# Kernel tuning notes

Hardware: AMD Instinct MI355X
Metric: run time of the kernel (lower is better)

Reference implementation:

```python
import jax, jax.numpy as jnp
import numpy as np
import math

B, T, C = 2, 2048, 1024
H, DK, DV = 16, 64, 64


def setup_inputs() -> dict:
    key = jax.random.key(0)
    ks = jax.random.split(key, 5)
    # randw(*d) = randn(*d) / sqrt(d[-1])
    x = jax.random.normal(ks[0], (B, T, C), dtype=jnp.float32)
    w_q = jax.random.normal(ks[1], (H, DK, C), dtype=jnp.float32) / math.sqrt(C)
    w_k = jax.random.normal(ks[2], (H, DK, C), dtype=jnp.float32) / math.sqrt(C)
    w_v = jax.random.normal(ks[3], (H, DV, C), dtype=jnp.float32) / math.sqrt(C)
    w_o = jax.random.normal(ks[4], (H * DV, C), dtype=jnp.float32) / math.sqrt(C)
    return {"x": x, "w_q": w_q, "w_k": w_k, "w_v": w_v, "w_o": w_o}


def reference(x, w_q, w_k, w_v, w_o):
    # Full prefill: bs_q.first = 0, bs_q.nb = T, causal=True, dropout=0 (eval).
    dk = w_q.shape[1]
    q = jnp.einsum('ntc,hdc->nhtd', x, w_q)  # [B,H,T,DK]
    k = jnp.einsum('ntc,hdc->nhtd', x, w_k)  # [B,H,T,DK]
    v = jnp.einsum('ntc,hdc->nhtd', x, w_v)  # [B,H,T,DV]
    a = jnp.einsum('nhtd,nhsd->nhts', q, k) / jnp.sqrt(jnp.asarray(dk, x.dtype))
    # amm_generator: mask where query_idx < key_idx (strict upper triangle)
    t = a.shape[-1]
    mask = jnp.arange(t)[:, None] < jnp.arange(t)[None, :]  # [T,T] bool
    a = jnp.where(mask[None, None], jnp.asarray(-jnp.inf, a.dtype), a)
    a = jax.nn.softmax(a, axis=-1)
    y = jnp.einsum('nhts,nhsd->nthd', a, v)  # [B,T,H,DV]
    y = y.reshape(y.shape[0], y.shape[1], -1)  # [B,T,H*DV]
    return y @ w_o  # [B,T,C]
```

## Files before the change

### kernel.cpp

```cpp
#include <hip/hip_runtime.h>
#include <hip/hip_bf16.h>

#define B_ 2
#define T_ 2048
#define C_ 1024
#define H_ 16
#define D_ 64

typedef __attribute__((ext_vector_type(8))) short bf16x8;
typedef __attribute__((ext_vector_type(4))) float f32x4;
typedef __attribute__((ext_vector_type(8))) unsigned short u16x8;
typedef __attribute__((ext_vector_type(2))) unsigned int u32x2;
typedef __attribute__((ext_vector_type(4))) unsigned int u32x4;

__device__ __forceinline__ unsigned short bf1(float a) {
    __bf16 x = (__bf16)a;
    return __builtin_bit_cast(unsigned short, x);
}
__device__ __forceinline__ unsigned int pk2(float a, float b) {
    return (unsigned int)bf1(a) | ((unsigned int)bf1(b) << 16);
}
__device__ __forceinline__ float bf2f(unsigned short u) {
    union { unsigned int u; float f; } v; v.u = (unsigned int)u << 16;
    return v.f;
}

__device__ __forceinline__ void gll16(const void* g, void* l) {
    __builtin_amdgcn_global_load_lds(
        (const __attribute__((address_space(1))) unsigned int*)g,
        (__attribute__((address_space(3))) unsigned int*)l, 16, 0, 0);
}

__global__ __launch_bounds__(256) void prep_x(
    const float* __restrict__ x, unsigned short* __restrict__ xb)
{
    const size_t i = ((size_t)blockIdx.x * 256 + threadIdx.x) * 16;
    float4 f0 = *reinterpret_cast<const float4*>(x + i);
    float4 f1 = *reinterpret_cast<const float4*>(x + i + 4);
    float4 f2 = *reinterpret_cast<const float4*>(x + i + 8);
    float4 f3 = *reinterpret_cast<const float4*>(x + i + 12);
    u32x4 a = {pk2(f0.x, f0.y), pk2(f0.z, f0.w), pk2(f1.x, f1.y), pk2(f1.z, f1.w)};
    u32x4 b = {pk2(f2.x, f2.y), pk2(f2.z, f2.w), pk2(f3.x, f3.y), pk2(f3.z, f3.w)};
    *reinterpret_cast<u32x4*>(xb + i) = a;
    *reinterpret_cast<u32x4*>(xb + i + 8) = b;
}

__global__ __launch_bounds__(256) void prep_w(
    const float* __restrict__ wq, const float* __restrict__ wk,
    const float* __restrict__ wv, unsigned short* __restrict__ wb)
{
    const int bid = blockIdx.x, tid = threadIdx.x;
    const int rb = bid * 4;
    const float* src = (rb < 1024) ? wq + (size_t)rb * 1024
                     : (rb < 2048) ? wk + (size_t)(rb - 1024) * 1024
                                   : wv + (size_t)(rb - 2048) * 1024;
    const float sc = (rb < 1024) ? 0.125f * 1.4426950408889634f : 1.0f;
    const float4* s4 = (const float4*)src;
    u32x2* d = (u32x2*)(wb + (size_t)rb * 1024);
#pragma unroll
    for (int k = 0; k < 4; k++) {
        float4 v = s4[k * 256 + tid];
        u32x2 w;
        w[0] = pk2(v.x * sc, v.y * sc);
        w[1] = pk2(v.z * sc, v.w * sc);
        d[k * 256 + tid] = w;
    }
}

__global__ __launch_bounds__(256) void prep_wo(
    const float* __restrict__ wo, unsigned short* __restrict__ wt)
{
    __shared__ unsigned short tile[64][72];
    const int tk = (blockIdx.x & 15) << 6, tn = (blockIdx.x >> 4) << 6;
    const int r = threadIdx.x >> 2, cb = (threadIdx.x & 3) << 4;
#pragma unroll
    for (int j = 0; j < 4; j++) {
        float4 v = *reinterpret_cast<const float4*>(
            wo + (size_t)(tk + r) * 1024 + tn + cb + j * 4);
        u32x2 w;
        w[0] = pk2(v.x, v.y);
        w[1] = pk2(v.z, v.w);
        *reinterpret_cast<u32x2*>(&tile[r][cb + j * 4]) = w;
    }
    __syncthreads();
    unsigned short buf[16];
#pragma unroll
    for (int j = 0; j < 16; j++) buf[j] = tile[cb + j][r];
    unsigned short* dst = wt + (size_t)(tn + r) * 1024 + tk + cb;
    *reinterpret_cast<u16x8*>(dst) = *reinterpret_cast<u16x8*>(buf);
    *reinterpret_cast<u16x8*>(dst + 8) = *reinterpret_cast<u16x8*>(buf + 8);
}

__global__ __launch_bounds__(256) void qkv_gemm(
    const unsigned short* __restrict__ xb, const unsigned short* __restrict__ wb,
    unsigned short* __restrict__ qkv)
{
    __shared__ __align__(16) unsigned short As[128 * 32];
    __shared__ __align__(16) unsigned short Bs[128 * 32];
    const int tid = threadIdx.x;
    const int lane = tid & 63, wave = tid >> 6;
    const int g = lane >> 4, c16 = lane & 15;
    const int xcd = blockIdx.x & 7, idx = blockIdx.x >> 3;
    const int bm = (xcd << 2) + idx / 24, bn = idx % 24;
    const int jbase = bn << 7;
    const int which = jbase >> 10;

    const int srow = lane >> 2, sch = (lane & 3) << 3;
    const unsigned short* asrc = xb + ((size_t)(bm << 7) + wave * 32 + srow) * C_ + sch;
    const unsigned short* bsrc = wb + ((size_t)(bn << 7) + wave * 32 + srow) * C_ + sch;

    f32x4 acc[4][4];
#pragma unroll
    for (int i = 0; i < 4; i++)
#pragma unroll
        for (int j = 0; j < 4; j++) acc[i][j] = (f32x4){0.f, 0.f, 0.f, 0.f};

    const int wm = (wave >> 1) << 6, wn = (wave & 1) << 6;

    for (int t = 0; t < 32; ++t) {
        const int k0 = t << 5;
        __syncthreads();
        gll16(asrc + k0,           &As[(wave * 32) << 5]);
        gll16(asrc + k0 + 16 * C_, &As[(wave * 32 + 16) << 5]);
        gll16(bsrc + k0,           &Bs[(wave * 32) << 5]);
        gll16(bsrc + k0 + 16 * C_, &Bs[(wave * 32 + 16) << 5]);
        __syncthreads();

        bf16x8 af[4], bfv[4];
#pragma unroll
        for (int m = 0; m < 4; m++)
            af[m] = *reinterpret_cast<const bf16x8*>(&As[((wm + m * 16 + c16) << 5) + g * 8]);
#pragma unroll
        for (int n = 0; n < 4; n++)
            bfv[n] = *reinterpret_cast<const bf16x8*>(&Bs[((wn + n * 16 + c16) << 5) + g * 8]);
#pragma unroll
        for (int m = 0; m < 4; m++)
#pragma unroll
            for (int n = 0; n < 4; n++)
                acc[m][n] = __builtin_amdgcn_mfma_f32_16x16x32_bf16(af[m], bfv[n], acc[m][n], 0, 0, 0);
    }

    if (which < 2) {
#pragma unroll
        for (int m = 0; m < 4; m++) {
            const int grow = (bm << 7) + wm + m * 16 + (g << 2);
#pragma unroll
            for (int n = 0; n < 4; n++) {
                const int jj = (jbase + wn + n * 16 + c16) & 1023;
                const int h = jj >> 6, d = jj & 63;
#pragma unroll
                for (int r = 0; r < 4; r++) {
                    const int row = grow + r;
                    const int b = row >> 11, t = row & 2047;
                    const size_t off = ((size_t)((which * B_ + b) * H_ + h) * T_ + t) * 64 + d;
                    qkv[off] = bf1(acc[m][n][r]);
                }
            }
        }
    } else {
#pragma unroll
        for (int m = 0; m < 4; m++) {
            const int grow = (bm << 7) + wm + m * 16 + (g << 2);
            const int b = grow >> 11, t = grow & 2047;
#pragma unroll
            for (int n = 0; n < 4; n++) {
                const int jj = (jbase + wn + n * 16 + c16) & 1023;
                const int h = jj >> 6, d = jj & 63;
                u32x2 w;
                w[0] = pk2(acc[m][n][0], acc[m][n][1]);
                w[1] = pk2(acc[m][n][2], acc[m][n][3]);
                const size_t off = ((size_t)((2 * B_ + b) * H_ + h) * 64 + d) * T_ + t;
                *reinterpret_cast<u32x2*>(&qkv[off]) = w;
            }
        }
    }
}

__global__ __launch_bounds__(256) void attn(
    const unsigned short* __restrict__ qkv,
    unsigned short* __restrict__ opA, unsigned short* __restrict__ opB,
    float* __restrict__ lbuf)
{
    __shared__ __align__(16) unsigned short Ks[2][64 * 64];
    __shared__ __align__(16) unsigned short Vt[2][64 * 64];
    __shared__ __align__(16) unsigned short Ps[4][16 * 64];
    const int tid = threadIdx.x, lane = tid & 63, wave = tid >> 6;
    const int g = lane >> 4, c16 = lane & 15;
    const int qt = 31 - (blockIdx.x >> 6);
    const int rem = blockIdx.x & 63;
    const int half = rem >> 5, bh = rem & 31;
    const int b = bh >> 4, h = bh & 15;
    const size_t headoff = (size_t)(b * H_ + h) * T_ * 64;
    const size_t QSZ = (size_t)B_ * H_ * T_ * 64;
    const unsigned short* qp = qkv + headoff;
    const unsigned short* kp = qkv + QSZ + headoff;
    const unsigned short* vTp = qkv + 2 * QSZ + headoff;

    const int nt = qt + 1;
    const int h1 = (nt + 1) >> 1;
    const int itlo = half ? h1 : 0, ithi = half ? nt : h1;

    const int qbase = (qt << 6) + wave * 16;
    bf16x8 qf0, qf1;
    {
        const size_t r0 = (size_t)(qbase + c16) * 64;
        qf0 = *reinterpret_cast<const bf16x8*>(qp + r0 + g * 8);
        qf1 = *reinterpret_cast<const bf16x8*>(qp + r0 + 32 + g * 8);
    }

    const bf16x8 ones = {0x3F80, 0x3F80, 0x3F80, 0x3F80, 0x3F80, 0x3F80, 0x3F80, 0x3F80};
    f32x4 lacc = (f32x4){0.f, 0.f, 0.f, 0.f};
    f32x4 acc[4];
#pragma unroll
    for (int i = 0; i < 4; i++) acc[i] = (f32x4){0.f, 0.f, 0.f, 0.f};

    const int srow8 = lane >> 3;
    const int swc = ((lane & 7) ^ srow8) << 3;
    const unsigned short* ksrc = kp + (size_t)(wave * 16 + srow8) * 64 + swc;
    const unsigned short* vsrc = vTp + (size_t)(wave * 16 + srow8) * T_ + swc;

    auto stage = [&](int buf, int s0) {
#pragma unroll
        for (int i = 0; i < 2; i++) {
            gll16(ksrc + (size_t)(s0 + i * 8) * 64, &Ks[buf][(wave * 16 + i * 8) << 6]);
            gll16(vsrc + s0 + (size_t)i * 8 * T_, &Vt[buf][(wave * 16 + i * 8) << 6]);
        }
    };

    if (itlo < ithi) {
        stage(0, itlo << 6);
        int cur = 0;
        for (int it = itlo; it < ithi; ++it) {
            __syncthreads();
            if (it + 1 < ithi) stage(cur ^ 1, (it + 1) << 6);
            const int s0 = it << 6;

            f32x4 sfT[4];
#pragma unroll
            for (int f = 0; f < 4; f++) sfT[f] = (f32x4){-16.f, -16.f, -16.f, -16.f};
            __builtin_amdgcn_s_setprio(1);
#pragma unroll
            for (int f = 0; f < 4; f++) {
                const int row = f * 16 + c16;
                const int sw = row & 7;
                bf16x8 k0 = *reinterpret_cast<const bf16x8*>(&Ks[cur][(row << 6) + ((g ^ sw) << 3)]);
                bf16x8 k1 = *reinterpret_cast<const bf16x8*>(&Ks[cur][(row << 6) + (((g + 4) ^ sw) << 3)]);
                sfT[f] = __builtin_amdgcn_mfma_f32_16x16x32_bf16(k0, qf0, sfT[f], 0, 0, 0);
                sfT[f] = __builtin_amdgcn_mfma_f32_16x16x32_bf16(k1, qf1, sfT[f], 0, 0, 0);
            }
            __builtin_amdgcn_s_setprio(0);

            if (it == qt) {
                const int qglob = qbase + c16;
#pragma unroll
                for (int f = 0; f < 4; f++)
#pragma unroll
                    for (int r = 0; r < 4; r++) {
                        const int kv = s0 + f * 16 + g * 4 + r;
                        if (kv > qglob) sfT[f][r] = -1e30f;
                    }
            }

#pragma unroll
            for (int f = 0; f < 4; f++)
#pragma unroll
                for (int r = 0; r < 4; r++)
                    sfT[f][r] = __builtin_amdgcn_exp2f(sfT[f][r]);

#pragma unroll
            for (int f = 0; f < 4; f++) {
                u32x2 w;
                w[0] = pk2(sfT[f][0], sfT[f][1]);
                w[1] = pk2(sfT[f][2], sfT[f][3]);
                const int addr = (c16 << 6) + ((((f << 1) + (g >> 1)) ^ (c16 & 7)) << 3) + ((g & 1) << 2);
                *reinterpret_cast<u32x2*>(&Ps[wave][addr]) = w;
            }

            __builtin_amdgcn_s_setprio(1);
#pragma unroll
            for (int ks = 0; ks < 2; ks++) {
                bf16x8 pa = *reinterpret_cast<const bf16x8*>(
                    &Ps[wave][(c16 << 6) + ((((ks << 2) + g) ^ (c16 & 7)) << 3)]);
                lacc = __builtin_amdgcn_mfma_f32_16x16x32_bf16(ones, pa, lacc, 0, 0, 0);
#pragma unroll
                for (int fd = 0; fd < 4; fd++) {
                    const int d = fd * 16 + c16;
                    bf16x8 vf = *reinterpret_cast<const bf16x8*>(
                        &Vt[cur][(d << 6) + ((((ks << 2) + g) ^ (d & 7)) << 3)]);
                    acc[fd] = __builtin_amdgcn_mfma_f32_16x16x32_bf16(vf, pa, acc[fd], 0, 0, 0);
                }
            }
            __builtin_amdgcn_s_setprio(0);
            cur ^= 1;
        }
    }

    unsigned short* op = half ? opB : opA;
#pragma unroll
    for (int fd = 0; fd < 4; fd++) {
        u32x2 w;
        w[0] = pk2(acc[fd][0], acc[fd][1]);
        w[1] = pk2(acc[fd][2], acc[fd][3]);
        const size_t cy = ((size_t)b * T_ + qbase + c16) * 1024 + h * 64 + fd * 16 + g * 4;
        *reinterpret_cast<u32x2*>(&op[cy]) = w;
    }
    if (lane < 16)
        lbuf[(size_t)half * (B_ * H_ * T_) + ((size_t)(b * H_ + h)) * T_ + qbase + c16] = lacc[0];
}

__global__ __launch_bounds__(256) void combine(
    const unsigned short* __restrict__ opA, const unsigned short* __restrict__ opB,
    const float* __restrict__ lbuf, unsigned short* __restrict__ y)
{
    const size_t i = ((size_t)blockIdx.x * 256 + threadIdx.x) * 8;
    const int hh = (int)((i >> 6) & 15);
    const int t = (int)((i >> 10) & 2047);
    const int bb = (int)(i >> 21);
    const size_t li = ((size_t)(bb * H_ + hh)) * T_ + t;
    const float inv = 1.0f / (lbuf[li] + lbuf[(size_t)B_ * H_ * T_ + li]);
    u16x8 a = *reinterpret_cast<const u16x8*>(opA + i);
    u16x8 c = *reinterpret_cast<const u16x8*>(opB + i);
    unsigned short o[8];
#pragma unroll
    for (int j = 0; j < 8; j++) o[j] = bf1((bf2f(a[j]) + bf2f(c[j])) * inv);
    *reinterpret_cast<u16x8*>(y + i) = *reinterpret_cast<u16x8*>(o);
}

__global__ __launch_bounds__(256) void out_proj(
    const unsigned short* __restrict__ y, const unsigned short* __restrict__ wt,
    float* __restrict__ out)
{
    __shared__ __align__(16) unsigned short As[128 * 32];
    __shared__ __align__(16) unsigned short Bs[64 * 32];
    const int tid = threadIdx.x;
    const int lane = tid & 63, wave = tid >> 6;
    const int g = lane >> 4, c16 = lane & 15;
    const int xcd = blockIdx.x & 7, idx = blockIdx.x >> 3;
    const int bm = (xcd << 2) + (idx >> 4), bn = idx & 15;
    const int wm = (wave >> 1) << 6, wn = (wave & 1) << 5;

    const int srow = lane >> 2, sch = (lane & 3) << 3;
    const unsigned short* ysrc = y + ((size_t)(bm << 7) + wave * 32 + srow) * 1024 + sch;
    const unsigned short* wsrc = wt + ((size_t)(bn << 6) + wave * 16 + srow) * 1024 + sch;

    f32x4 acc[4][2];
#pragma unroll
    for (int i = 0; i < 4; i++)
#pragma unroll
        for (int j = 0; j < 2; j++) acc[i][j] = (f32x4){0.f, 0.f, 0.f, 0.f};

    for (int t = 0; t < 32; ++t) {
        const int k0 = t << 5;
        __syncthreads();
        gll16(ysrc + k0,            &As[(wave * 32) << 5]);
        gll16(ysrc + k0 + 16 * 1024, &As[(wave * 32 + 16) << 5]);
        gll16(wsrc + k0,            &Bs[(wave * 16) << 5]);
        __syncthreads();

        bf16x8 af[4], bfr[2];
#pragma unroll
        for (int m = 0; m < 4; m++)
            af[m] = *reinterpret_cast<const bf16x8*>(&As[((wm + m * 16 + c16) << 5) + g * 8]);
#pragma unroll
        for (int n = 0; n < 2; n++)
            bfr[n] = *reinterpret_cast<const bf16x8*>(&Bs[((wn + n * 16 + c16) << 5) + g * 8]);
#pragma unroll
        for (int m = 0; m < 4; m++)
#pragma unroll
            for (int n = 0; n < 2; n++)
                acc[m][n] = __builtin_amdgcn_mfma_f32_16x16x32_bf16(af[m], bfr[n], acc[m][n], 0, 0, 0);
    }

#pragma unroll
    for (int m = 0; m < 4; m++) {
        const int grow = (bm << 7) + wm + m * 16 + (g << 2);
#pragma unroll
        for (int n = 0; n < 2; n++) {
            const int gcol = (bn << 6) + wn + n * 16 + c16;
#pragma unroll
            for (int r = 0; r < 4; r++)
                out[(size_t)(grow + r) * 1024 + gcol] = acc[m][n][r];
        }
    }
}

extern "C" void kernel_launch(void* const* d_in, const int* in_sizes, int n_in,
                              void* d_out, int out_size, void* d_ws, size_t ws_size,
                              hipStream_t stream) {
    const float* x  = (const float*)d_in[0];
    const float* wq = (const float*)d_in[1];
    const float* wk = (const float*)d_in[2];
    const float* wv = (const float*)d_in[3];
    const float* wo = (const float*)d_in[4];
    float* out = (float*)d_out;

    unsigned short* wb   = (unsigned short*)d_ws;
    unsigned short* opB  = (unsigned short*)d_ws;
    unsigned short* y    = opB;
    unsigned short* qkv  = (unsigned short*)d_ws + (size_t)4 * 1024 * 1024;
    unsigned short* wt   = qkv;
    unsigned short* xb   = (unsigned short*)d_out;
    unsigned short* opA  = (unsigned short*)d_out;
    float* lbuf = (float*)((char*)d_out + (size_t)8 * 1024 * 1024);

    prep_x<<<dim3(1024), 256, 0, stream>>>(x, xb);
    prep_w<<<dim3(768), 256, 0, stream>>>(wq, wk, wv, wb);
    qkv_gemm<<<dim3(768), 256, 0, stream>>>(xb, wb, qkv);
    attn<<<dim3(2048), 256, 0, stream>>>(qkv, opA, opB, lbuf);
    combine<<<dim3(4096), 256, 0, stream>>>(opA, opB, lbuf, y);
    prep_wo<<<dim3(256), 256, 0, stream>>>(wo, wt);
    out_proj<<<dim3(512), 256, 0, stream>>>(y, wt, out);
}
```

Before: 116.8 us.

## Merge prep and combine kernels, single-buffer attention K/V tiles

Merges the x and weight conversion kernels into one launch, and merges the combine step with the w_o transpose-convert into another, cutting two kernel launches. The combine grid shrinks to exactly cover the output, so the old extra blocks that did redundant work go away. The attention kernel drops K/V double buffering for a single LDS buffer with barriers around each load, and precomputes the swizzled LDS read and write addresses. Halving the attention LDS may raise occupancy, but loads no longer overlap with compute within a block.

```diff
diff --git a/kernel.cpp b/kernel.cpp
--- a/kernel.cpp
+++ b/kernel.cpp
@@ -31,64 +31,39 @@
         (__attribute__((address_space(3))) unsigned int*)l, 16, 0, 0);
 }
 
-__global__ __launch_bounds__(256) void prep_x(
-    const float* __restrict__ x, unsigned short* __restrict__ xb)
-{
-    const size_t i = ((size_t)blockIdx.x * 256 + threadIdx.x) * 16;
-    float4 f0 = *reinterpret_cast<const float4*>(x + i);
-    float4 f1 = *reinterpret_cast<const float4*>(x + i + 4);
-    float4 f2 = *reinterpret_cast<const float4*>(x + i + 8);
-    float4 f3 = *reinterpret_cast<const float4*>(x + i + 12);
-    u32x4 a = {pk2(f0.x, f0.y), pk2(f0.z, f0.w), pk2(f1.x, f1.y), pk2(f1.z, f1.w)};
-    u32x4 b = {pk2(f2.x, f2.y), pk2(f2.z, f2.w), pk2(f3.x, f3.y), pk2(f3.z, f3.w)};
-    *reinterpret_cast<u32x4*>(xb + i) = a;
-    *reinterpret_cast<u32x4*>(xb + i + 8) = b;
-}
-
-__global__ __launch_bounds__(256) void prep_w(
-    const float* __restrict__ wq, const float* __restrict__ wk,
-    const float* __restrict__ wv, unsigned short* __restrict__ wb)
+__global__ __launch_bounds__(256) void prep_all(
+    const float* __restrict__ x, const float* __restrict__ wq,
+    const float* __restrict__ wk, const float* __restrict__ wv,
+    unsigned short* __restrict__ xb, unsigned short* __restrict__ wb)
 {
     const int bid = blockIdx.x, tid = threadIdx.x;
-    const int rb = bid * 4;
-    const float* src = (rb < 1024) ? wq + (size_t)rb * 1024
-                     : (rb < 2048) ? wk + (size_t)(rb - 1024) * 1024
-                                   : wv + (size_t)(rb - 2048) * 1024;
-    const float sc = (rb < 1024) ? 0.125f * 1.4426950408889634f : 1.0f;
-    const float4* s4 = (const float4*)src;
-    u32x2* d = (u32x2*)(wb + (size_t)rb * 1024);
-#pragma unroll
-    for (int k = 0; k < 4; k++) {
-        float4 v = s4[k * 256 + tid];
-        u32x2 w;
-        w[0] = pk2(v.x * sc, v.y * sc);
-        w[1] = pk2(v.z * sc, v.w * sc);
-        d[k * 256 + tid] = w;
-    }
-}
-
-__global__ __launch_bounds__(256) void prep_wo(
-    const float* __restrict__ wo, unsigned short* __restrict__ wt)
-{
-    __shared__ unsigned short tile[64][72];
-    const int tk = (blockIdx.x & 15) << 6, tn = (blockIdx.x >> 4) << 6;
-    const int r = threadIdx.x >> 2, cb = (threadIdx.x & 3) << 4;
-#pragma unroll
-    for (int j = 0; j < 4; j++) {
-        float4 v = *reinterpret_cast<const float4*>(
-            wo + (size_t)(tk + r) * 1024 + tn + cb + j * 4);
-        u32x2 w;
-        w[0] = pk2(v.x, v.y);
-        w[1] = pk2(v.z, v.w);
-        *reinterpret_cast<u32x2*>(&tile[r][cb + j * 4]) = w;
-    }
-    __syncthreads();
-    unsigned short buf[16];
-#pragma unroll
-    for (int j = 0; j < 16; j++) buf[j] = tile[cb + j][r];
-    unsigned short* dst = wt + (size_t)(tn + r) * 1024 + tk + cb;
-    *reinterpret_cast<u16x8*>(dst) = *reinterpret_cast<u16x8*>(buf);
-    *reinterpret_cast<u16x8*>(dst + 8) = *reinterpret_cast<u16x8*>(buf + 8);
+    if (bid < 1024) {
+        const size_t i = ((size_t)bid * 256 + tid) * 16;
+        float4 f0 = *reinterpret_cast<const float4*>(x + i);
+        float4 f1 = *reinterpret_cast<const float4*>(x + i + 4);
+        float4 f2 = *reinterpret_cast<const float4*>(x + i + 8);
+        float4 f3 = *reinterpret_cast<const float4*>(x + i + 12);
+        u32x4 a = {pk2(f0.x, f0.y), pk2(f0.z, f0.w), pk2(f1.x, f1.y), pk2(f1.z, f1.w)};
+        u32x4 b = {pk2(f2.x, f2.y), pk2(f2.z, f2.w), pk2(f3.x, f3.y), pk2(f3.z, f3.w)};
+        *reinterpret_cast<u32x4*>(xb + i) = a;
+        *reinterpret_cast<u32x4*>(xb + i + 8) = b;
+    } else {
+        const int rb = (bid - 1024) * 4;
+        const float* src = (rb < 1024) ? wq + (size_t)rb * 1024
+                         : (rb < 2048) ? wk + (size_t)(rb - 1024) * 1024
+                                       : wv + (size_t)(rb - 2048) * 1024;
+        const float sc = (rb < 1024) ? 0.125f * 1.4426950408889634f : 1.0f;
+        const float4* s4 = (const float4*)src;
+        u32x2* d = (u32x2*)(wb + (size_t)rb * 1024);
+#pragma unroll
+        for (int k = 0; k < 4; k++) {
+            float4 v = s4[k * 256 + tid];
+            u32x2 w;
+            w[0] = pk2(v.x * sc, v.y * sc);
+            w[1] = pk2(v.z * sc, v.w * sc);
+            d[k * 256 + tid] = w;
+        }
+    }
 }
 
 __global__ __launch_bounds__(256) void qkv_gemm(
@@ -181,8 +156,8 @@
     unsigned short* __restrict__ opA, unsigned short* __restrict__ opB,
     float* __restrict__ lbuf)
 {
-    __shared__ __align__(16) unsigned short Ks[2][64 * 64];
-    __shared__ __align__(16) unsigned short Vt[2][64 * 64];
+    __shared__ __align__(16) unsigned short Ks[64 * 64];
+    __shared__ __align__(16) unsigned short Vt[64 * 64];
     __shared__ __align__(16) unsigned short Ps[4][16 * 64];
     const int tid = threadIdx.x, lane = tid & 63, wave = tid >> 6;
     const int g = lane >> 4, c16 = lane & 15;
@@ -200,10 +175,10 @@
     const int h1 = (nt + 1) >> 1;
     const int itlo = half ? h1 : 0, ithi = half ? nt : h1;
 
-    const int qbase = (qt << 6) + wave * 16;
+    const int qb = (qt << 6) + wave * 16;
     bf16x8 qf0, qf1;
     {
-        const size_t r0 = (size_t)(qbase + c16) * 64;
+        const size_t r0 = (size_t)(qb + c16) * 64;
         qf0 = *reinterpret_cast<const bf16x8*>(qp + r0 + g * 8);
         qf1 = *reinterpret_cast<const bf16x8*>(qp + r0 + 32 + g * 8);
     }
@@ -213,86 +188,88 @@
     f32x4 acc[4];
 #pragma unroll
     for (int i = 0; i < 4; i++) acc[i] = (f32x4){0.f, 0.f, 0.f, 0.f};
+
+    const int sw = c16 & 7;
+    const int rdo0 = (c16 << 6) + ((g ^ sw) << 3);
+    const int rdo1 = (c16 << 6) + (((g + 4) ^ sw) << 3);
+    const unsigned short* kr0 = Ks + rdo0;
+    const unsigned short* kr1 = Ks + rdo1;
+    const unsigned short* vr0 = Vt + rdo0;
+    const unsigned short* vr1 = Vt + rdo1;
+    const unsigned short* par0 = Ps[wave] + rdo0;
+    const unsigned short* par1 = Ps[wave] + rdo1;
+    unsigned short* pw[4];
+#pragma unroll
+    for (int f = 0; f < 4; f++)
+        pw[f] = Ps[wave] + (c16 << 6)
+              + (((((f << 1) + (g >> 1))) ^ sw) << 3) + ((g & 1) << 2);
 
     const int srow8 = lane >> 3;
     const int swc = ((lane & 7) ^ srow8) << 3;
     const unsigned short* ksrc = kp + (size_t)(wave * 16 + srow8) * 64 + swc;
     const unsigned short* vsrc = vTp + (size_t)(wave * 16 + srow8) * T_ + swc;
 
-    auto stage = [&](int buf, int s0) {
+    for (int it = itlo; it < ithi; ++it) {
+        const int s0 = it << 6;
+        __syncthreads();
 #pragma unroll
         for (int i = 0; i < 2; i++) {
-            gll16(ksrc + (size_t)(s0 + i * 8) * 64, &Ks[buf][(wave * 16 + i * 8) << 6]);
-            gll16(vsrc + s0 + (size_t)i * 8 * T_, &Vt[buf][(wave * 16 + i * 8) << 6]);
-        }
-    };
-
-    if (itlo < ithi) {
-        stage(0, itlo << 6);
-        int cur = 0;
-        for (int it = itlo; it < ithi; ++it) {
-            __syncthreads();
-            if (it + 1 < ithi) stage(cur ^ 1, (it + 1) << 6);
-            const int s0 = it << 6;
-
-            f32x4 sfT[4];
-#pragma unroll
-            for (int f = 0; f < 4; f++) sfT[f] = (f32x4){-16.f, -16.f, -16.f, -16.f};
-            __builtin_amdgcn_s_setprio(1);
-#pragma unroll
-            for (int f = 0; f < 4; f++) {
-                const int row = f * 16 + c16;
-                const int sw = row & 7;
-                bf16x8 k0 = *reinterpret_cast<const bf16x8*>(&Ks[cur][(row << 6) + ((g ^ sw) << 3)]);
-                bf16x8 k1 = *reinterpret_cast<const bf16x8*>(&Ks[cur][(row << 6) + (((g + 4) ^ sw) << 3)]);
-                sfT[f] = __builtin_amdgcn_mfma_f32_16x16x32_bf16(k0, qf0, sfT[f], 0, 0, 0);
-                sfT[f] = __builtin_amdgcn_mfma_f32_16x16x32_bf16(k1, qf1, sfT[f], 0, 0, 0);
+            gll16(ksrc + (size_t)(s0 + i * 8) * 64, &Ks[(wave * 16 + i * 8) << 6]);
+            gll16(vsrc + s0 + (size_t)i * 8 * T_, &Vt[(wave * 16 + i * 8) << 6]);
+        }
+        __syncthreads();
+
+        f32x4 sfT[4];
+#pragma unroll
+        for (int f = 0; f < 4; f++) sfT[f] = (f32x4){-16.f, -16.f, -16.f, -16.f};
+        __builtin_amdgcn_s_setprio(1);
+#pragma unroll
+        for (int f = 0; f < 4; f++) {
+            bf16x8 k0 = *reinterpret_cast<const bf16x8*>(kr0 + f * 1024);
+            bf16x8 k1 = *reinterpret_cast<const bf16x8*>(kr1 + f * 1024);
+            sfT[f] = __builtin_amdgcn_mfma_f32_16x16x32_bf16(k0, qf0, sfT[f], 0, 0, 0);
+            sfT[f] = __builtin_amdgcn_mfma_f32_16x16x32_bf16(k1, qf1, sfT[f], 0, 0, 0);
+        }
+        __builtin_amdgcn_s_setprio(0);
+
+        if (it == qt) {
+            const int qg = qb + c16;
+#pragma unroll
+            for (int f = 0; f < 4; f++)
+#pragma unroll
+                for (int r = 0; r < 4; r++) {
+                    const int kv = s0 + f * 16 + g * 4 + r;
+                    if (kv > qg) sfT[f][r] = -1e30f;
+                }
+        }
+
+#pragma unroll
+        for (int f = 0; f < 4; f++)
+#pragma unroll
+            for (int r = 0; r < 4; r++)
+                sfT[f][r] = __builtin_amdgcn_exp2f(sfT[f][r]);
+
+#pragma unroll
+        for (int f = 0; f < 4; f++) {
+            u32x2 w;
+            w[0] = pk2(sfT[f][0], sfT[f][1]);
+            w[1] = pk2(sfT[f][2], sfT[f][3]);
+            *reinterpret_cast<u32x2*>(pw[f]) = w;
+        }
+
+        __builtin_amdgcn_s_setprio(1);
+#pragma unroll
+        for (int ks = 0; ks < 2; ks++) {
+            bf16x8 pa = *reinterpret_cast<const bf16x8*>(ks ? par1 : par0);
+            const unsigned short* vp = ks ? vr1 : vr0;
+            lacc = __builtin_amdgcn_mfma_f32_16x16x32_bf16(ones, pa, lacc, 0, 0, 0);
+#pragma unroll
+            for (int fd = 0; fd < 4; fd++) {
+                bf16x8 vf = *reinterpret_cast<const bf16x8*>(vp + fd * 1024);
+                acc[fd] = __builtin_amdgcn_mfma_f32_16x16x32_bf16(vf, pa, acc[fd], 0, 0, 0);
             }
-            __builtin_amdgcn_s_setprio(0);
-
-            if (it == qt) {
-                const int qglob = qbase + c16;
-#pragma unroll
-                for (int f = 0; f < 4; f++)
-#pragma unroll
-                    for (int r = 0; r < 4; r++) {
-                        const int kv = s0 + f * 16 + g * 4 + r;
-                        if (kv > qglob) sfT[f][r] = -1e30f;
-                    }
-            }
-
-#pragma unroll
-            for (int f = 0; f < 4; f++)
-#pragma unroll
-                for (int r = 0; r < 4; r++)
-                    sfT[f][r] = __builtin_amdgcn_exp2f(sfT[f][r]);
-
-#pragma unroll
-            for (int f = 0; f < 4; f++) {
-                u32x2 w;
-                w[0] = pk2(sfT[f][0], sfT[f][1]);
-                w[1] = pk2(sfT[f][2], sfT[f][3]);
-                const int addr = (c16 << 6) + ((((f << 1) + (g >> 1)) ^ (c16 & 7)) << 3) + ((g & 1) << 2);
-                *reinterpret_cast<u32x2*>(&Ps[wave][addr]) = w;
-            }
-
-            __builtin_amdgcn_s_setprio(1);
-#pragma unroll
-            for (int ks = 0; ks < 2; ks++) {
-                bf16x8 pa = *reinterpret_cast<const bf16x8*>(
-                    &Ps[wave][(c16 << 6) + ((((ks << 2) + g) ^ (c16 & 7)) << 3)]);
-                lacc = __builtin_amdgcn_mfma_f32_16x16x32_bf16(ones, pa, lacc, 0, 0, 0);
-#pragma unroll
-                for (int fd = 0; fd < 4; fd++) {
-                    const int d = fd * 16 + c16;
-                    bf16x8 vf = *reinterpret_cast<const bf16x8*>(
-                        &Vt[cur][(d << 6) + ((((ks << 2) + g) ^ (d & 7)) << 3)]);
-                    acc[fd] = __builtin_amdgcn_mfma_f32_16x16x32_bf16(vf, pa, acc[fd], 0, 0, 0);
-                }
-            }
-            __builtin_amdgcn_s_setprio(0);
-            cur ^= 1;
-        }
+        }
+        __builtin_amdgcn_s_setprio(0);
     }
 
     unsigned short* op = half ? opB : opA;
@@ -301,29 +278,54 @@
         u32x2 w;
         w[0] = pk2(acc[fd][0], acc[fd][1]);
         w[1] = pk2(acc[fd][2], acc[fd][3]);
-        const size_t cy = ((size_t)b * T_ + qbase + c16) * 1024 + h * 64 + fd * 16 + g * 4;
+        const size_t cy = ((size_t)b * T_ + qb + c16) * 1024 + h * 64 + fd * 16 + g * 4;
         *reinterpret_cast<u32x2*>(&op[cy]) = w;
     }
     if (lane < 16)
-        lbuf[(size_t)half * (B_ * H_ * T_) + ((size_t)(b * H_ + h)) * T_ + qbase + c16] = lacc[0];
-}
-
-__global__ __launch_bounds__(256) void combine(
+        lbuf[(size_t)half * (B_ * H_ * T_) + ((size_t)(b * H_ + h)) * T_ + qb + c16] = lacc[0];
+}
+
+__global__ __launch_bounds__(256) void combine_wo(
     const unsigned short* __restrict__ opA, const unsigned short* __restrict__ opB,
-    const float* __restrict__ lbuf, unsigned short* __restrict__ y)
+    const float* __restrict__ lbuf, unsigned short* __restrict__ y,
+    const float* __restrict__ wo, unsigned short* __restrict__ wt)
 {
-    const size_t i = ((size_t)blockIdx.x * 256 + threadIdx.x) * 8;
-    const int hh = (int)((i >> 6) & 15);
-    const int t = (int)((i >> 10) & 2047);
-    const int bb = (int)(i >> 21);
-    const size_t li = ((size_t)(bb * H_ + hh)) * T_ + t;
-    const float inv = 1.0f / (lbuf[li] + lbuf[(size_t)B_ * H_ * T_ + li]);
-    u16x8 a = *reinterpret_cast<const u16x8*>(opA + i);
-    u16x8 c = *reinterpret_cast<const u16x8*>(opB + i);
-    unsigned short o[8];
-#pragma unroll
-    for (int j = 0; j < 8; j++) o[j] = bf1((bf2f(a[j]) + bf2f(c[j])) * inv);
-    *reinterpret_cast<u16x8*>(y + i) = *reinterpret_cast<u16x8*>(o);
+    __shared__ unsigned short tile[64][72];
+    const int bid = blockIdx.x, tid = threadIdx.x;
+    if (bid < 2048) {
+        const size_t i = ((size_t)bid * 256 + tid) * 8;
+        const int hh = (int)((i >> 6) & 15);
+        const int t = (int)((i >> 10) & 2047);
+        const int bb = (int)(i >> 21);
+        const size_t li = ((size_t)(bb * H_ + hh)) * T_ + t;
+        const float inv = 1.0f / (lbuf[li] + lbuf[(size_t)B_ * H_ * T_ + li]);
+        u16x8 a = *reinterpret_cast<const u16x8*>(opA + i);
+        u16x8 c = *reinterpret_cast<const u16x8*>(opB + i);
+        unsigned short o[8];
+#pragma unroll
+        for (int j = 0; j < 8; j++) o[j] = bf1((bf2f(a[j]) + bf2f(c[j])) * inv);
+        *reinterpret_cast<u16x8*>(y + i) = *reinterpret_cast<u16x8*>(o);
+    } else {
+        const int wb2 = bid - 2048;
+        const int tk = (wb2 & 15) << 6, tn = (wb2 >> 4) << 6;
+        const int r = tid >> 2, cb = (tid & 3) << 4;
+#pragma unroll
+        for (int j = 0; j < 4; j++) {
+            float4 v = *reinterpret_cast<const float4*>(
+                wo + (size_t)(tk + r) * 1024 + tn + cb + j * 4);
+            u32x2 w;
+            w[0] = pk2(v.x, v.y);
+            w[1] = pk2(v.z, v.w);
+            *reinterpret_cast<u32x2*>(&tile[r][cb + j * 4]) = w;
+        }
+        __syncthreads();
+        unsigned short buf[16];
+#pragma unroll
+        for (int j = 0; j < 16; j++) buf[j] = tile[cb + j][r];
+        unsigned short* dst = wt + (size_t)(tn + r) * 1024 + tk + cb;
+        *reinterpret_cast<u16x8*>(dst) = *reinterpret_cast<u16x8*>(buf);
+        *reinterpret_cast<u16x8*>(dst + 8) = *reinterpret_cast<u16x8*>(buf + 8);
+    }
 }
 
 __global__ __launch_bounds__(256) void out_proj(
@@ -352,9 +354,9 @@
     for (int t = 0; t < 32; ++t) {
         const int k0 = t << 5;
         __syncthreads();
-        gll16(ysrc + k0,            &As[(wave * 32) << 5]);
+        gll16(ysrc + k0,             &As[(wave * 32) << 5]);
         gll16(ysrc + k0 + 16 * 1024, &As[(wave * 32 + 16) << 5]);
-        gll16(wsrc + k0,            &Bs[(wave * 16) << 5]);
+        gll16(wsrc + k0,             &Bs[(wave * 16) << 5]);
         __syncthreads();
 
         bf16x8 af[4], bfr[2];
@@ -403,11 +405,9 @@
     unsigned short* opA  = (unsigned short*)d_out;
     float* lbuf = (float*)((char*)d_out + (size_t)8 * 1024 * 1024);
 
-    prep_x<<<dim3(1024), 256, 0, stream>>>(x, xb);
-    prep_w<<<dim3(768), 256, 0, stream>>>(wq, wk, wv, wb);
+    prep_all<<<dim3(1792), 256, 0, stream>>>(x, wq, wk, wv, xb, wb);
     qkv_gemm<<<dim3(768), 256, 0, stream>>>(xb, wb, qkv);
     attn<<<dim3(2048), 256, 0, stream>>>(qkv, opA, opB, lbuf);
-    combine<<<dim3(4096), 256, 0, stream>>>(opA, opB, lbuf, y);
-    prep_wo<<<dim3(256), 256, 0, stream>>>(wo, wt);
+    combine_wo<<<dim3(2048 + 256), 256, 0, stream>>>(opA, opB, lbuf, y, wo, wt);
     out_proj<<<dim3(512), 256, 0, stream>>>(y, wt, out);
 }
```

Result: faster. 107.5 us (median of 2 runs) (-7.9%).
